# Optimization experiments

Hardware: AMD Instinct MI355X
Metric: run time of the kernel (lower is better)

The kernel has to match this reference:

```python
import jax, jax.numpy as jnp
import numpy as np

SCALES = (4, 8, 16, 32)
EPS = 1e-12  # F.normalize clamp_min eps


def _segments(x, scale):
    """Sliding-window segments per timestep, zero-padded at the end to `scale`.
    Replicates torch: start=max(0,j-scale//2+1), end=min(j+scale//2, T) slice,
    then cat over j along dim 0 -> [T*B, scale, D]."""
    B, T, D = x.shape
    j = jnp.arange(T)
    start = jnp.maximum(0, j - scale // 2 + 1)            # [T]
    last = jnp.minimum(j + scale // 2, T - 1)             # last valid index
    idx = start[:, None] + jnp.arange(scale)[None, :]     # [T, scale]
    mask = idx <= last[:, None]                           # valid (non-pad) slots
    seg = x[:, jnp.clip(idx, 0, T - 1), :]                # [B, T, scale, D]
    seg = seg * mask[None, :, :, None].astype(x.dtype)
    # torch.cat over j (dim 0) of [B, scale, D] blocks -> index t*B + b
    return jnp.transpose(seg, (1, 0, 2, 3)).reshape(T * B, scale, D)


def setup_inputs() -> dict:
    key = jax.random.key(0)
    ks = jax.random.split(key, 1 + len(SCALES))
    B, T, D = 4, 1024, 512
    inp = {"x": jax.random.normal(ks[0], (B, T, D), dtype=jnp.float32)}
    for i, s in enumerate(SCALES):
        # nn.Linear(s, 4, bias=False): weight [4, s], kaiming-uniform-ish init
        bound = 1.0 / np.sqrt(s)
        inp[f"W{i}"] = jax.random.uniform(ks[1 + i], (4, s), dtype=jnp.float32,
                                          minval=-bound, maxval=bound)
    return inp


def reference(x, W0, W1, W2, W3):
    Ws = (W0, W1, W2, W3)
    outs = []
    for s, W in zip(SCALES, Ws):
        seg = _segments(x, s)                                     # [TB, s, D]
        n = jnp.sqrt(jnp.sum(seg * seg, axis=-1, keepdims=True))  # L2 over D
        seg = seg / jnp.maximum(n, EPS)                           # F.normalize(dim=-1)
        # permute -> [TB, D, s]; Linear(s->4); permute back -> [TB, 4, D]
        y = jnp.einsum('nsd,os->nod', seg, W)
        outs.append(y)
    # all scales map to 4 output channels -> identical shapes; stack the list
    return jnp.stack(outs, axis=0)  # [n_scales, T*B, 4, D]
```

## Files before the change

kernel.cpp:

```cpp
#include <hip/hip_runtime.h>

#define T_DIM 1024
#define B_DIM 4
#define D_DIM 512
#define DQ (D_DIM / 4)
#define NROWS (T_DIM * B_DIM)
#define SSTR ((size_t)NROWS * 4 * DQ)

__global__ __launch_bounds__(256) void norm_kernel(const float* __restrict__ x,
                                                   float* __restrict__ inv) {
    const int wave = threadIdx.x >> 6;
    const int lane = threadIdx.x & 63;
    const int row  = blockIdx.x * 4 + wave;
    const float4* xr = reinterpret_cast<const float4*>(x) + (size_t)row * DQ;
    float4 a = xr[lane];
    float4 c = xr[lane + 64];
    float s2 = a.x*a.x + a.y*a.y + a.z*a.z + a.w*a.w
             + c.x*c.x + c.y*c.y + c.z*c.z + c.w*c.w;
    #pragma unroll
    for (int off = 32; off > 0; off >>= 1) s2 += __shfl_xor(s2, off, 64);
    if (lane == 0) inv[row] = 1.0f / fmaxf(sqrtf(s2), 1e-12f);
}

__device__ __forceinline__ void fma4(float4& a, float wt, const float4& v) {
    a.x += wt * v.x; a.y += wt * v.y; a.z += wt * v.z; a.w += wt * v.w;
}

template<int S>
__device__ __forceinline__ void gen_scale(const float* __restrict__ W,
                                          const float4* __restrict__ xq,
                                          const float* __restrict__ inv,
                                          int j, int b,
                                          float4& a0, float4& a1,
                                          float4& a2, float4& a3) {
    const int lo = max(0, j - S / 2 + 1);
    const int hi = min(j + S / 2, T_DIM - 1);
    for (int t = lo; t <= hi; ++t) {
        float4 xv = xq[(size_t)t * DQ];
        const float s = inv[b * T_DIM + t];
        xv.x *= s; xv.y *= s; xv.z *= s; xv.w *= s;
        const int kk = t - lo;
        fma4(a0, W[0 * S + kk], xv);
        fma4(a1, W[1 * S + kk], xv);
        fma4(a2, W[2 * S + kk], xv);
        fma4(a3, W[3 * S + kk], xv);
    }
}

__global__ __launch_bounds__(128) void pool_kernel(const float* __restrict__ x,
                                                   const float* __restrict__ inv,
                                                   const float* __restrict__ W0,
                                                   const float* __restrict__ W1,
                                                   const float* __restrict__ W2,
                                                   const float* __restrict__ W3,
                                                   float* __restrict__ out) {
    const int bid = (blockIdx.x & 7) * (NROWS / 8) + (blockIdx.x >> 3);
    const int j = bid & (T_DIM - 1);
    const int b = bid >> 10;
    const int n = j * B_DIM + b;
    const int dq = threadIdx.x;
    const float4* xq  = reinterpret_cast<const float4*>(x) + (size_t)b * T_DIM * DQ + dq;
    float4* outq      = reinterpret_cast<float4*>(out) + (size_t)n * 4 * DQ + dq;

    float4 acc[16];
    #pragma unroll
    for (int i = 0; i < 16; ++i) acc[i] = make_float4(0.f, 0.f, 0.f, 0.f);

    if (j >= 15 && j <= T_DIM - 17) {
        __shared__ float sinv[32];
        const int t0 = j - 15;
        if (threadIdx.x < 32) sinv[threadIdx.x] = inv[b * T_DIM + t0 + threadIdx.x];
        __syncthreads();
        #pragma unroll
        for (int k = 0; k < 32; ++k) {
            float4 xv = xq[(size_t)(t0 + k) * DQ];
            const float s = sinv[k];
            xv.x *= s; xv.y *= s; xv.z *= s; xv.w *= s;
            if (k >= 14 && k < 18) {
                #pragma unroll
                for (int o = 0; o < 4; ++o) fma4(acc[0 + o], W0[o * 4 + (k - 14)], xv);
            }
            if (k >= 12 && k < 20) {
                #pragma unroll
                for (int o = 0; o < 4; ++o) fma4(acc[4 + o], W1[o * 8 + (k - 12)], xv);
            }
            if (k >= 8 && k < 24) {
                #pragma unroll
                for (int o = 0; o < 4; ++o) fma4(acc[8 + o], W2[o * 16 + (k - 8)], xv);
            }
            {
                #pragma unroll
                for (int o = 0; o < 4; ++o) fma4(acc[12 + o], W3[o * 32 + k], xv);
            }
        }
    } else {
        gen_scale<4 >(W0, xq, inv, j, b, acc[0],  acc[1],  acc[2],  acc[3]);
        gen_scale<8 >(W1, xq, inv, j, b, acc[4],  acc[5],  acc[6],  acc[7]);
        gen_scale<16>(W2, xq, inv, j, b, acc[8],  acc[9],  acc[10], acc[11]);
        gen_scale<32>(W3, xq, inv, j, b, acc[12], acc[13], acc[14], acc[15]);
    }

    #pragma unroll
    for (int si = 0; si < 4; ++si)
        #pragma unroll
        for (int o = 0; o < 4; ++o)
            outq[(size_t)si * SSTR + (size_t)o * DQ] = acc[si * 4 + o];
}

extern "C" void kernel_launch(void* const* d_in, const int* in_sizes, int n_in,
                              void* d_out, int out_size, void* d_ws, size_t ws_size,
                              hipStream_t stream) {
    const float* x  = (const float*)d_in[0];
    const float* W0 = (const float*)d_in[1];
    const float* W1 = (const float*)d_in[2];
    const float* W2 = (const float*)d_in[3];
    const float* W3 = (const float*)d_in[4];
    float* out = (float*)d_out;
    float* inv = (float*)d_ws;

    norm_kernel<<<NROWS / 4, 256, 0, stream>>>(x, inv);
    pool_kernel<<<NROWS, 128, 0, stream>>>(x, inv, W0, W1, W2, W3, out);
}
```

Baseline: 46.90 us.

## Tile eight timesteps per block with pre-normalized LDS window and nontemporal stores

Each block now handles 8 consecutive timesteps and stages a 39-row pre-normalized window of x in shared memory, so the 32-row windows of neighbouring timesteps reuse the same loads instead of each reading from global memory. The normalization scale is applied once per row during staging rather than per use. Output stores switch to nontemporal writes to avoid polluting cache with the large write-only output. The trade-off is about 80KB of LDS per block, which limits occupancy, plus fewer and larger blocks.

```diff
diff --git a/kernel.cpp b/kernel.cpp
--- a/kernel.cpp
+++ b/kernel.cpp
@@ -6,6 +6,16 @@
 #define DQ (D_DIM / 4)
 #define NROWS (T_DIM * B_DIM)
 #define SSTR ((size_t)NROWS * 4 * DQ)
+#define JT 8
+#define NTILES (NROWS / JT)
+#define ROWS_ST (JT + 31)
+
+typedef float f32x4 __attribute__((ext_vector_type(4)));
+
+__device__ __forceinline__ void nt_store4(const float4& v, float4* p) {
+    __builtin_nontemporal_store(*reinterpret_cast<const f32x4*>(&v),
+                                reinterpret_cast<f32x4*>(p));
+}
 
 __global__ __launch_bounds__(256) void norm_kernel(const float* __restrict__ x,
                                                    float* __restrict__ inv) {
@@ -31,8 +41,7 @@
                                           const float4* __restrict__ xq,
                                           const float* __restrict__ inv,
                                           int j, int b,
-                                          float4& a0, float4& a1,
-                                          float4& a2, float4& a3) {
+                                          float4* acc) {
     const int lo = max(0, j - S / 2 + 1);
     const int hi = min(j + S / 2, T_DIM - 1);
     for (int t = lo; t <= hi; ++t) {
@@ -40,71 +49,96 @@
         const float s = inv[b * T_DIM + t];
         xv.x *= s; xv.y *= s; xv.z *= s; xv.w *= s;
         const int kk = t - lo;
-        fma4(a0, W[0 * S + kk], xv);
-        fma4(a1, W[1 * S + kk], xv);
-        fma4(a2, W[2 * S + kk], xv);
-        fma4(a3, W[3 * S + kk], xv);
+        fma4(acc[0], W[0 * S + kk], xv);
+        fma4(acc[1], W[1 * S + kk], xv);
+        fma4(acc[2], W[2 * S + kk], xv);
+        fma4(acc[3], W[3 * S + kk], xv);
     }
 }
 
-__global__ __launch_bounds__(128) void pool_kernel(const float* __restrict__ x,
+__global__ __launch_bounds__(256) void pool_kernel(const float* __restrict__ x,
                                                    const float* __restrict__ inv,
                                                    const float* __restrict__ W0,
                                                    const float* __restrict__ W1,
                                                    const float* __restrict__ W2,
                                                    const float* __restrict__ W3,
                                                    float* __restrict__ out) {
-    const int bid = (blockIdx.x & 7) * (NROWS / 8) + (blockIdx.x >> 3);
-    const int j = bid & (T_DIM - 1);
-    const int b = bid >> 10;
-    const int n = j * B_DIM + b;
-    const int dq = threadIdx.x;
-    const float4* xq  = reinterpret_cast<const float4*>(x) + (size_t)b * T_DIM * DQ + dq;
-    float4* outq      = reinterpret_cast<float4*>(out) + (size_t)n * 4 * DQ + dq;
+    __shared__ float4 xs[ROWS_ST * DQ];
+    const int tile = (blockIdx.x & 7) * (NTILES / 8) + (blockIdx.x >> 3);
+    const int b  = tile >> 7;
+    const int j0 = (tile & 127) * JT;
+    const int q  = threadIdx.x & 127;
+    const int jg = threadIdx.x >> 7;
+    const float4* xqb = reinterpret_cast<const float4*>(x) + (size_t)b * T_DIM * DQ;
 
-    float4 acc[16];
-    #pragma unroll
-    for (int i = 0; i < 16; ++i) acc[i] = make_float4(0.f, 0.f, 0.f, 0.f);
+    if (j0 >= 16) {
+        for (int l = jg; l < ROWS_ST; l += 2) {
+            const int t = j0 - 15 + l;
+            float4 v = make_float4(0.f, 0.f, 0.f, 0.f);
+            if (t < T_DIM) {
+                v = xqb[(size_t)t * DQ + q];
+                const float s = inv[b * T_DIM + t];
+                v.x *= s; v.y *= s; v.z *= s; v.w *= s;
+            }
+            xs[l * DQ + q] = v;
+        }
+        __syncthreads();
 
-    if (j >= 15 && j <= T_DIM - 17) {
-        __shared__ float sinv[32];
-        const int t0 = j - 15;
-        if (threadIdx.x < 32) sinv[threadIdx.x] = inv[b * T_DIM + t0 + threadIdx.x];
-        __syncthreads();
-        #pragma unroll
-        for (int k = 0; k < 32; ++k) {
-            float4 xv = xq[(size_t)(t0 + k) * DQ];
-            const float s = sinv[k];
-            xv.x *= s; xv.y *= s; xv.z *= s; xv.w *= s;
-            if (k >= 14 && k < 18) {
+        for (int jj = 0; jj < 4; ++jj) {
+            const int u = jg * 4 + jj;
+            const int j = j0 + u;
+            const float4* xrow = &xs[u * DQ + q];
+            float4 acc[16];
+            #pragma unroll
+            for (int i = 0; i < 16; ++i) acc[i] = make_float4(0.f, 0.f, 0.f, 0.f);
+            #pragma unroll
+            for (int k = 0; k < 32; ++k) {
+                const float4 xv = xrow[k * DQ];
+                if (k >= 14 && k < 18) {
+                    #pragma unroll
+                    for (int o = 0; o < 4; ++o) fma4(acc[0 + o], W0[o * 4 + (k - 14)], xv);
+                }
+                if (k >= 12 && k < 20) {
+                    #pragma unroll
+                    for (int o = 0; o < 4; ++o) fma4(acc[4 + o], W1[o * 8 + (k - 12)], xv);
+                }
+                if (k >= 8 && k < 24) {
+                    #pragma unroll
+                    for (int o = 0; o < 4; ++o) fma4(acc[8 + o], W2[o * 16 + (k - 8)], xv);
+                }
+                {
+                    #pragma unroll
+                    for (int o = 0; o < 4; ++o) fma4(acc[12 + o], W3[o * 32 + k], xv);
+                }
+            }
+            const int n = j * B_DIM + b;
+            float4* outq = reinterpret_cast<float4*>(out) + (size_t)n * 4 * DQ + q;
+            #pragma unroll
+            for (int si = 0; si < 4; ++si)
                 #pragma unroll
-                for (int o = 0; o < 4; ++o) fma4(acc[0 + o], W0[o * 4 + (k - 14)], xv);
-            }
-            if (k >= 12 && k < 20) {
-                #pragma unroll
-                for (int o = 0; o < 4; ++o) fma4(acc[4 + o], W1[o * 8 + (k - 12)], xv);
-            }
-            if (k >= 8 && k < 24) {
-                #pragma unroll
-                for (int o = 0; o < 4; ++o) fma4(acc[8 + o], W2[o * 16 + (k - 8)], xv);
-            }
-            {
-                #pragma unroll
-                for (int o = 0; o < 4; ++o) fma4(acc[12 + o], W3[o * 32 + k], xv);
-            }
+                for (int o = 0; o < 4; ++o)
+                    nt_store4(acc[si * 4 + o], &outq[(size_t)si * SSTR + (size_t)o * DQ]);
         }
     } else {
-        gen_scale<4 >(W0, xq, inv, j, b, acc[0],  acc[1],  acc[2],  acc[3]);
-        gen_scale<8 >(W1, xq, inv, j, b, acc[4],  acc[5],  acc[6],  acc[7]);
-        gen_scale<16>(W2, xq, inv, j, b, acc[8],  acc[9],  acc[10], acc[11]);
-        gen_scale<32>(W3, xq, inv, j, b, acc[12], acc[13], acc[14], acc[15]);
+        const float4* xq = xqb + q;
+        for (int jj = 0; jj < 4; ++jj) {
+            const int j = j0 + jg * 4 + jj;
+            float4 acc[16];
+            #pragma unroll
+            for (int i = 0; i < 16; ++i) acc[i] = make_float4(0.f, 0.f, 0.f, 0.f);
+            gen_scale<4 >(W0, xq, inv, j, b, &acc[0]);
+            gen_scale<8 >(W1, xq, inv, j, b, &acc[4]);
+            gen_scale<16>(W2, xq, inv, j, b, &acc[8]);
+            gen_scale<32>(W3, xq, inv, j, b, &acc[12]);
+            const int n = j * B_DIM + b;
+            float4* outq = reinterpret_cast<float4*>(out) + (size_t)n * 4 * DQ + q;
+            #pragma unroll
+            for (int si = 0; si < 4; ++si)
+                #pragma unroll
+                for (int o = 0; o < 4; ++o)
+                    nt_store4(acc[si * 4 + o], &outq[(size_t)si * SSTR + (size_t)o * DQ]);
+        }
     }
-
-    #pragma unroll
-    for (int si = 0; si < 4; ++si)
-        #pragma unroll
-        for (int o = 0; o < 4; ++o)
-            outq[(size_t)si * SSTR + (size_t)o * DQ] = acc[si * 4 + o];
 }
 
 extern "C" void kernel_launch(void* const* d_in, const int* in_sizes, int n_in,
@@ -119,5 +153,5 @@
     float* inv = (float*)d_ws;
 
     norm_kernel<<<NROWS / 4, 256, 0, stream>>>(x, inv);
-    pool_kernel<<<NROWS, 128, 0, stream>>>(x, inv, W0, W1, W2, W3, out);
+    pool_kernel<<<NTILES, 256, 0, stream>>>(x, inv, W0, W1, W2, W3, out);
 }
```

Result: faster. 45.63 us (-2.7%).

## Process two timesteps for all batches per 512-thread block in pool kernel

Applied to the files above, without the earlier changes.

Each pool block now has 512 threads, one 128-thread group per batch element, and loops over two adjacent timesteps. The grid drops from 4096 to 512 blocks. The aim is to amortise the inverse-norm shared-memory load and the block launch over more output, and to let the second timestep's window reuse x rows in cache. The cost is fewer blocks in flight to hide memory latency, a serial per-thread loop over the two timesteps, and possible register pressure under launch_bounds(512,4).

```diff
diff --git a/kernel.cpp b/kernel.cpp
--- a/kernel.cpp
+++ b/kernel.cpp
@@ -6,6 +6,7 @@
 #define DQ (D_DIM / 4)
 #define NROWS (T_DIM * B_DIM)
 #define SSTR ((size_t)NROWS * 4 * DQ)
+#define NB 512
 
 __global__ __launch_bounds__(256) void norm_kernel(const float* __restrict__ x,
                                                    float* __restrict__ inv) {
@@ -31,8 +32,7 @@
                                           const float4* __restrict__ xq,
                                           const float* __restrict__ inv,
                                           int j, int b,
-                                          float4& a0, float4& a1,
-                                          float4& a2, float4& a3) {
+                                          float4* acc) {
     const int lo = max(0, j - S / 2 + 1);
     const int hi = min(j + S / 2, T_DIM - 1);
     for (int t = lo; t <= hi; ++t) {
@@ -40,71 +40,78 @@
         const float s = inv[b * T_DIM + t];
         xv.x *= s; xv.y *= s; xv.z *= s; xv.w *= s;
         const int kk = t - lo;
-        fma4(a0, W[0 * S + kk], xv);
-        fma4(a1, W[1 * S + kk], xv);
-        fma4(a2, W[2 * S + kk], xv);
-        fma4(a3, W[3 * S + kk], xv);
+        fma4(acc[0], W[0 * S + kk], xv);
+        fma4(acc[1], W[1 * S + kk], xv);
+        fma4(acc[2], W[2 * S + kk], xv);
+        fma4(acc[3], W[3 * S + kk], xv);
     }
 }
 
-__global__ __launch_bounds__(128) void pool_kernel(const float* __restrict__ x,
-                                                   const float* __restrict__ inv,
-                                                   const float* __restrict__ W0,
-                                                   const float* __restrict__ W1,
-                                                   const float* __restrict__ W2,
-                                                   const float* __restrict__ W3,
-                                                   float* __restrict__ out) {
-    const int bid = (blockIdx.x & 7) * (NROWS / 8) + (blockIdx.x >> 3);
-    const int j = bid & (T_DIM - 1);
-    const int b = bid >> 10;
-    const int n = j * B_DIM + b;
-    const int dq = threadIdx.x;
-    const float4* xq  = reinterpret_cast<const float4*>(x) + (size_t)b * T_DIM * DQ + dq;
-    float4* outq      = reinterpret_cast<float4*>(out) + (size_t)n * 4 * DQ + dq;
+__global__ __launch_bounds__(512, 4) void pool_kernel(const float* __restrict__ x,
+                                                      const float* __restrict__ inv,
+                                                      const float* __restrict__ W0,
+                                                      const float* __restrict__ W1,
+                                                      const float* __restrict__ W2,
+                                                      const float* __restrict__ W3,
+                                                      float* __restrict__ out) {
+    const int g  = (blockIdx.x & 7) * (NB / 8) + (blockIdx.x >> 3);
+    const int j0 = g * 2;
+    const int q  = threadIdx.x & 127;
+    const int b  = threadIdx.x >> 7;
+    const float4* xqb = reinterpret_cast<const float4*>(x) + (size_t)b * T_DIM * DQ;
 
-    float4 acc[16];
-    #pragma unroll
-    for (int i = 0; i < 16; ++i) acc[i] = make_float4(0.f, 0.f, 0.f, 0.f);
+    const bool interior = (j0 >= 16) && (j0 <= T_DIM - 18);
+    __shared__ float sinv[B_DIM][36];
+    if (interior && q < 33)
+        sinv[b][q] = inv[b * T_DIM + (j0 - 15) + q];
+    __syncthreads();
 
-    if (j >= 15 && j <= T_DIM - 17) {
-        __shared__ float sinv[32];
-        const int t0 = j - 15;
-        if (threadIdx.x < 32) sinv[threadIdx.x] = inv[b * T_DIM + t0 + threadIdx.x];
-        __syncthreads();
+    #pragma unroll 1
+    for (int jj = 0; jj < 2; ++jj) {
+        const int j = j0 + jj;
+        float4 acc[16];
         #pragma unroll
-        for (int k = 0; k < 32; ++k) {
-            float4 xv = xq[(size_t)(t0 + k) * DQ];
-            const float s = sinv[k];
-            xv.x *= s; xv.y *= s; xv.z *= s; xv.w *= s;
-            if (k >= 14 && k < 18) {
-                #pragma unroll
-                for (int o = 0; o < 4; ++o) fma4(acc[0 + o], W0[o * 4 + (k - 14)], xv);
+        for (int i = 0; i < 16; ++i) acc[i] = make_float4(0.f, 0.f, 0.f, 0.f);
+
+        if (interior) {
+            const int t0 = j - 15;
+            #pragma unroll
+            for (int k = 0; k < 32; ++k) {
+                float4 xv = xqb[(size_t)(t0 + k) * DQ + q];
+                const float s = sinv[b][jj + k];
+                xv.x *= s; xv.y *= s; xv.z *= s; xv.w *= s;
+                if (k >= 14 && k < 18) {
+                    #pragma unroll
+                    for (int o = 0; o < 4; ++o) fma4(acc[0 + o], W0[o * 4 + (k - 14)], xv);
+                }
+                if (k >= 12 && k < 20) {
+                    #pragma unroll
+                    for (int o = 0; o < 4; ++o) fma4(acc[4 + o], W1[o * 8 + (k - 12)], xv);
+                }
+                if (k >= 8 && k < 24) {
+                    #pragma unroll
+                    for (int o = 0; o < 4; ++o) fma4(acc[8 + o], W2[o * 16 + (k - 8)], xv);
+                }
+                {
+                    #pragma unroll
+                    for (int o = 0; o < 4; ++o) fma4(acc[12 + o], W3[o * 32 + k], xv);
+                }
             }
-            if (k >= 12 && k < 20) {
-                #pragma unroll
-                for (int o = 0; o < 4; ++o) fma4(acc[4 + o], W1[o * 8 + (k - 12)], xv);
-            }
-            if (k >= 8 && k < 24) {
-                #pragma unroll
-                for (int o = 0; o < 4; ++o) fma4(acc[8 + o], W2[o * 16 + (k - 8)], xv);
-            }
-            {
-                #pragma unroll
-                for (int o = 0; o < 4; ++o) fma4(acc[12 + o], W3[o * 32 + k], xv);
-            }
+        } else {
+            gen_scale<4 >(W0, xqb + q, inv, j, b, &acc[0]);
+            gen_scale<8 >(W1, xqb + q, inv, j, b, &acc[4]);
+            gen_scale<16>(W2, xqb + q, inv, j, b, &acc[8]);
+            gen_scale<32>(W3, xqb + q, inv, j, b, &acc[12]);
         }
-    } else {
-        gen_scale<4 >(W0, xq, inv, j, b, acc[0],  acc[1],  acc[2],  acc[3]);
-        gen_scale<8 >(W1, xq, inv, j, b, acc[4],  acc[5],  acc[6],  acc[7]);
-        gen_scale<16>(W2, xq, inv, j, b, acc[8],  acc[9],  acc[10], acc[11]);
-        gen_scale<32>(W3, xq, inv, j, b, acc[12], acc[13], acc[14], acc[15]);
+
+        const int n = j * B_DIM + b;
+        float4* outq = reinterpret_cast<float4*>(out) + (size_t)n * 4 * DQ + q;
+        #pragma unroll
+        for (int si = 0; si < 4; ++si)
+            #pragma unroll
+            for (int o = 0; o < 4; ++o)
+                outq[(size_t)si * SSTR + (size_t)o * DQ] = acc[si * 4 + o];
     }
-
-    #pragma unroll
-    for (int si = 0; si < 4; ++si)
-        #pragma unroll
-        for (int o = 0; o < 4; ++o)
-            outq[(size_t)si * SSTR + (size_t)o * DQ] = acc[si * 4 + o];
 }
 
 extern "C" void kernel_launch(void* const* d_in, const int* in_sizes, int n_in,
@@ -119,5 +126,5 @@
     float* inv = (float*)d_ws;
 
     norm_kernel<<<NROWS / 4, 256, 0, stream>>>(x, inv);
-    pool_kernel<<<NROWS, 128, 0, stream>>>(x, inv, W0, W1, W2, W3, out);
+    pool_kernel<<<NB, 512, 0, stream>>>(x, inv, W0, W1, W2, W3, out);
 }
```

After: 56.21 us. 19.8% more time.
